# Optimization experiments

Measured on AMD Instinct MI355X. Metric: run time of the kernel, lower is better.

Reference implementation:

```python
import jax, jax.numpy as jnp
import numpy as np

BN_EPS = 1e-3
SLOPE = 0.1
K = 100
CLUSTER_TEMP = 5.0


def setup_inputs() -> dict:
    key = jax.random.key(0)
    ks = jax.random.split(key, 5)
    N, Cin, Cout = 8192, 1, 64
    d = 49 * Cout  # (28/4)^2 * out_channels
    return {
        "x": jax.random.normal(ks[0], (N, Cin, 28, 28), jnp.float32),
        "conv1_w": jax.random.normal(ks[1], (128, Cin, 5, 5), jnp.float32) * 0.05,
        "conv1_b": jnp.zeros((128,), jnp.float32),
        "bn1_gamma": jnp.ones((128,), jnp.float32),
        "bn1_beta": jnp.zeros((128,), jnp.float32),
        "bn1_mean": jnp.zeros((128,), jnp.float32),
        "bn1_var": jnp.ones((128,), jnp.float32),
        "conv2_w": jax.random.normal(ks[2], (Cout, 128, 5, 5), jnp.float32) * 0.02,
        "conv2_b": jnp.zeros((Cout,), jnp.float32),
        "bn2_gamma": jnp.ones((Cout,), jnp.float32),
        "bn2_beta": jnp.zeros((Cout,), jnp.float32),
        "bn2_mean": jnp.zeros((Cout,), jnp.float32),
        "bn2_var": jnp.ones((Cout,), jnp.float32),
        "init_mu": jax.random.uniform(ks[3], (K, d), jnp.float32),
        "num_iter": 10,
    }


def _conv_bn_lrelu(x, w, b, gamma, beta, mean, var):
    # Conv2d(k=5, s=2, p=2) -> BatchNorm (eval/running stats) -> LeakyReLU(0.1)
    h = jax.lax.conv_general_dilated(
        x, w, window_strides=(2, 2), padding=[(2, 2), (2, 2)],
        dimension_numbers=("NCHW", "OIHW", "NCHW"))
    h = h + b[None, :, None, None]
    inv = gamma * jax.lax.rsqrt(var + BN_EPS)
    h = h * inv[None, :, None, None] + (beta - mean * inv)[None, :, None, None]
    return jnp.where(h >= 0, h, SLOPE * h)


def _cluster(data, mu, num_iter):
    # Row L2-normalize (equivalent to diag(1/||row||) @ data)
    data = data / jnp.linalg.norm(data, axis=1, keepdims=True)  # [n, d]
    for _ in range(num_iter):
        dist = data @ mu.T                                 # [n, K]
        r = jax.nn.softmax(CLUSTER_TEMP * dist, axis=1)    # [n, K]
        cluster_r = r.sum(axis=0)                          # [K]
        cluster_mean = r.T @ data                          # [K, d]
        mu = cluster_mean / cluster_r[:, None]
    dist = data @ mu.T
    r = jax.nn.softmax(CLUSTER_TEMP * dist, axis=1)
    return mu, r, dist


def reference(x, conv1_w, conv1_b, bn1_gamma, bn1_beta, bn1_mean, bn1_var,
              conv2_w, conv2_b, bn2_gamma, bn2_beta, bn2_mean, bn2_var,
              init_mu, num_iter):
    h = _conv_bn_lrelu(x, conv1_w, conv1_b, bn1_gamma, bn1_beta, bn1_mean, bn1_var)
    h = _conv_bn_lrelu(h, conv2_w, conv2_b, bn2_gamma, bn2_beta, bn2_mean, bn2_var)
    embeds = h.reshape(h.shape[0], -1)                     # [N, 49*Cout]
    mu_init, _, _ = _cluster(embeds, init_mu, int(num_iter))
    mu, r, dist = _cluster(embeds, jax.lax.stop_gradient(mu_init), 1)
    return mu, r, dist
```

## Files before the change

### kernel.cpp

```cpp
#include <hip/hip_runtime.h>
#include <hip/hip_bf16.h>
#include <math.h>

#define BN_EPS 1e-3f
#define SLOPE  0.1f
#define TEMP   5.0f
#define DDIM   3136
#define DDIMP  3200

typedef __attribute__((ext_vector_type(8))) short bf16x8;
typedef __attribute__((ext_vector_type(4))) float f32x4;

static __device__ __forceinline__ short f2b(float f) {
  __hip_bfloat16 h = __float2bfloat16(f);
  return *reinterpret_cast<short*>(&h);
}

#define W2B_OFF   0u
#define W1B_OFF   102400u
#define DB_OFF    204800u
#define DB_SZ     (8192u*3136u/2u)
#define DT_OFF    (DB_OFF + DB_SZ)
#define DT_SZ     (3200u*8192u/2u)
#define MUB_OFF   (DT_OFF + DT_SZ)
#define MUB_SZ    (112u*3136u/2u)
#define MUF_OFF   (MUB_OFF + MUB_SZ)
#define MUF_SZ    (100u*3136u)
#define CMS_OFF   (MUF_OFF + MUF_SZ)
#define CMS_SZ    (16u*3200u*112u/2u)
#define RT_OFF    (CMS_OFF + CMS_SZ)
#define RT_SZ     (112u*8192u/2u)
#define CR_OFF    (RT_OFF + RT_SZ)

__global__ __launch_bounds__(256) void k_w2b(const float* __restrict__ w2,
                                             __hip_bfloat16* __restrict__ w2b) {
  int idx = blockIdx.x * 256 + threadIdx.x;
  if (idx >= 204800) return;
  int ci   = idx & 31;
  int lr   = (idx >> 5) & 15;
  int rest = idx >> 9;
  int kk   = rest % 100;
  int oct  = rest / 100;
  int oc   = oct * 16 + lr;
  int tap  = kk >> 2;
  int c    = ((kk & 3) << 5) + ci;
  w2b[idx] = __float2bfloat16(w2[(oc * 128 + c) * 25 + tap]);
}

__global__ __launch_bounds__(256) void k_w1b(const float* __restrict__ w1,
                                             __hip_bfloat16* __restrict__ w1b) {
  int idx = blockIdx.x * 256 + threadIdx.x;
  if (idx >= 4096) return;
  int k   = idx & 31;
  int lr  = (idx >> 5) & 15;
  int oct = idx >> 9;
  int oc  = oct * 16 + lr;
  float v = (k < 25) ? w1[oc * 25 + k] : 0.f;
  w1b[idx] = __float2bfloat16(v);
}

__global__ __launch_bounds__(256) void k_conv(
    const float* __restrict__ x,
    const __hip_bfloat16* __restrict__ w1bh, const float* __restrict__ b1,
    const float* __restrict__ g1,  const float* __restrict__ be1,
    const float* __restrict__ mn1, const float* __restrict__ vr1,
    const __hip_bfloat16* __restrict__ w2bh, const float* __restrict__ b2,
    const float* __restrict__ g2,  const float* __restrict__ be2,
    const float* __restrict__ mn2, const float* __restrict__ vr2,
    __hip_bfloat16* __restrict__ db) {
  __shared__ float xs[1024];
  __shared__ float bn2s[128];
  __shared__ float bn1a[128], bn1b[128];
  __shared__ float nrm[4];
  __shared__ __align__(16) __hip_bfloat16 h1s[197 * 128];

  const int t    = threadIdx.x;
  const int img  = blockIdx.x;
  const int lane = t & 63;
  const int wv   = t >> 6;
  const int lr   = lane & 15;
  const int kg   = lane >> 4;
  const short* w2b = (const short*)w2bh;
  const short* w1b = (const short*)w1bh;

  for (int i = t; i < 1024; i += 256) xs[i] = 0.f;
  if (t < 64) {
    float a2 = g2[t] * rsqrtf(vr2[t] + BN_EPS);
    bn2s[t]      = a2;
    bn2s[64 + t] = b2[t] * a2 + be2[t] - mn2[t] * a2;
    ((unsigned*)(h1s + 196 * 128))[t] = 0u;
  }
  if (t < 128) {
    float a1 = g1[t] * rsqrtf(vr1[t] + BN_EPS);
    bn1a[t] = a1;
    bn1b[t] = b1[t] * a1 + be1[t] - mn1[t] * a1;
  }
  __syncthreads();
  const float* xi = x + (size_t)img * 784;
  for (int i = t; i < 784; i += 256) {
    int yy = i / 28, xx = i % 28;
    xs[(yy + 2) * 32 + (xx + 2)] = xi[i];
  }
  __syncthreads();

  {
    bf16x8 a0 = *(const bf16x8*)(w1b + (2 * wv) * 512 + lr * 32 + kg * 8);
    bf16x8 a1 = *(const bf16x8*)(w1b + (2 * wv + 1) * 512 + lr * 32 + kg * 8);
    for (int pt = 0; pt < 13; ++pt) {
      const int px  = pt * 16 + lr;
      const int pxc = (px < 196) ? px : 195;
      const int oy  = pxc / 14, ox = pxc - 14 * (pxc / 14);
      const float* xb = xs + (2 * oy) * 32 + 2 * ox;
      short bs[8];
#pragma unroll
      for (int j = 0; j < 8; ++j) {
        int k   = kg * 8 + j;
        int tap = (k < 25) ? k : 0;
        int kh  = tap / 5, kw = tap - 5 * (tap / 5);
        bs[j] = f2b(xb[kh * 32 + kw]);
      }
      bf16x8 b;
#pragma unroll
      for (int j = 0; j < 8; ++j) b[j] = bs[j];
      f32x4 c0 = {0.f, 0.f, 0.f, 0.f}, c1 = {0.f, 0.f, 0.f, 0.f};
      c0 = __builtin_amdgcn_mfma_f32_16x16x32_bf16(a0, b, c0, 0, 0, 0);
      c1 = __builtin_amdgcn_mfma_f32_16x16x32_bf16(a1, b, c1, 0, 0, 0);
      if (px < 196) {
        const int swz = (px & 7) << 4;
        unsigned w0lo, w0hi, w1lo, w1hi;
        {
          float v[4], u[4];
#pragma unroll
          for (int r = 0; r < 4; ++r) {
            int oc = wv * 32 + kg * 4 + r;
            float h = c0[r] * bn1a[oc] + bn1b[oc];
            v[r] = (h >= 0.f) ? h : SLOPE * h;
            int oc2 = oc + 16;
            float h2 = c1[r] * bn1a[oc2] + bn1b[oc2];
            u[r] = (h2 >= 0.f) ? h2 : SLOPE * h2;
          }
          w0lo = (unsigned)(unsigned short)f2b(v[0]) |
                 ((unsigned)(unsigned short)f2b(v[1]) << 16);
          w0hi = (unsigned)(unsigned short)f2b(v[2]) |
                 ((unsigned)(unsigned short)f2b(v[3]) << 16);
          w1lo = (unsigned)(unsigned short)f2b(u[0]) |
                 ((unsigned)(unsigned short)f2b(u[1]) << 16);
          w1hi = (unsigned)(unsigned short)f2b(u[2]) |
                 ((unsigned)(unsigned short)f2b(u[3]) << 16);
        }
        char* base = (char*)h1s + px * 256;
        const int o0 = ((wv * 32 + kg * 4) * 2) ^ swz;
        const int o1 = ((wv * 32 + 16 + kg * 4) * 2) ^ swz;
        *(uint2*)(base + o0) = make_uint2(w0lo, w0hi);
        *(uint2*)(base + o1) = make_uint2(w1lo, w1hi);
      }
    }
  }
  __syncthreads();

  const int woff  = lr * 32 + kg * 8;
  const int kgoff = kg << 4;
  int pxA[4], oyA[4], oxA[4];
#pragma unroll
  for (int pt = 0; pt < 4; ++pt) {
    int p = pt * 16 + lr;
    pxA[pt] = p;
    oyA[pt] = p / 7;
    oxA[pt] = p - 7 * oyA[pt];
  }

  f32x4 acc[4][4];
#pragma unroll
  for (int oct = 0; oct < 4; ++oct)
#pragma unroll
    for (int pt = 0; pt < 4; ++pt) acc[oct][pt] = (f32x4){0.f, 0.f, 0.f, 0.f};

  const int s0 = 25 * wv, s1e = s0 + 25;
  int curtap = -1;
  int rowB[4], rowS[4];

  auto loadk = [&](int kk, bf16x8* areg, bf16x8* breg) {
    int tap = kk >> 2;
    if (tap != curtap) {
      curtap = tap;
      int kh = tap / 5, kw = tap - 5 * (tap / 5);
#pragma unroll
      for (int pt = 0; pt < 4; ++pt) {
        int iy = 2 * oyA[pt] - 2 + kh;
        int ix = 2 * oxA[pt] - 2 + kw;
        bool val = (pxA[pt] < 49) & ((unsigned)iy < 14u) & ((unsigned)ix < 14u);
        int ip = val ? iy * 14 + ix : 196;
        rowB[pt] = ip * 256;
        rowS[pt] = (ip & 7) << 4;
      }
    }
    int c01 = (kk & 3) << 6;
#pragma unroll
    for (int oct = 0; oct < 4; ++oct)
      areg[oct] = *(const bf16x8*)(w2b + ((oct * 100 + kk) << 9) + woff);
#pragma unroll
    for (int pt = 0; pt < 4; ++pt)
      breg[pt] = *(const bf16x8*)((const char*)h1s + rowB[pt] +
                                  ((c01 | kgoff) ^ rowS[pt]));
  };

  bf16x8 a[4], b[4], an[4], bn_[4];
  loadk(s0, a, b);
  for (int kk = s0; kk < s1e; ++kk) {
    if (kk + 1 < s1e) loadk(kk + 1, an, bn_);
#pragma unroll
    for (int oct = 0; oct < 4; ++oct)
#pragma unroll
      for (int pt = 0; pt < 4; ++pt)
        acc[oct][pt] = __builtin_amdgcn_mfma_f32_16x16x32_bf16(a[oct], b[pt],
                                                               acc[oct][pt], 0, 0, 0);
#pragma unroll
    for (int q = 0; q < 4; ++q) { a[q] = an[q]; b[q] = bn_[q]; }
  }
  __syncthreads();

  float* red = (float*)h1s;
  if (wv != 0) {
#pragma unroll
    for (int oct = 0; oct < 4; ++oct)
#pragma unroll
      for (int pt = 0; pt < 4; ++pt)
#pragma unroll
        for (int r = 0; r < 4; ++r)
          red[(wv - 1) * 4096 + ((oct * 4 + pt) * 4 + r) * 64 + lane] =
              acc[oct][pt][r];
  }
  __syncthreads();
  if (wv == 0) {
#pragma unroll
    for (int oct = 0; oct < 4; ++oct)
#pragma unroll
      for (int pt = 0; pt < 4; ++pt)
#pragma unroll
        for (int r = 0; r < 4; ++r) {
          const int i = (oct * 4 + pt) * 4 + r;
          float v = acc[oct][pt][r] + red[i * 64 + lane] +
                    red[4096 + i * 64 + lane] + red[8192 + i * 64 + lane];
          red[i * 64 + lane] = v;
        }
  }
  __syncthreads();

  float outv[16];
  float ss = 0.f;
#pragma unroll
  for (int pt = 0; pt < 4; ++pt) {
#pragma unroll
    for (int r = 0; r < 4; ++r) {
      const int i = ((wv * 4 + pt) * 4 + r);
      float v = red[i * 64 + lane];
      const int oc = wv * 16 + kg * 4 + r;
      v = v * bn2s[oc] + bn2s[64 + oc];
      v = (v >= 0.f) ? v : SLOPE * v;
      outv[pt * 4 + r] = v;
      if (pxA[pt] < 49) ss += v * v;
    }
  }
#pragma unroll
  for (int m = 1; m < 64; m <<= 1) ss += __shfl_xor(ss, m, 64);
  if (lane == 0) nrm[wv] = ss;
  __syncthreads();
  const float invn = rsqrtf(nrm[0] + nrm[1] + nrm[2] + nrm[3]);
  __hip_bfloat16* dro = db + (size_t)img * DDIM;
#pragma unroll
  for (int pt = 0; pt < 4; ++pt) {
    if (pxA[pt] < 49) {
#pragma unroll
      for (int r = 0; r < 4; ++r) {
        const int oc = wv * 16 + kg * 4 + r;
        dro[oc * 49 + pxA[pt]] = __float2bfloat16(outv[pt * 4 + r] * invn);
      }
    }
  }
}

__global__ __launch_bounds__(256) void k_tr(const __hip_bfloat16* __restrict__ dbh,
                                            __hip_bfloat16* __restrict__ dTh) {
  __shared__ short tile[64][72];
  const int t   = threadIdx.x;
  const int i   = t >> 2;
  const int seg = t & 3;
  const size_t img0 = (size_t)blockIdx.x * 64;
  const size_t d0   = (size_t)blockIdx.y * 64;
  const short* src = (const short*)dbh + (img0 + i) * DDIM + d0 + seg * 16;
  bf16x8 v0 = *(const bf16x8*)src;
  bf16x8 v1 = *(const bf16x8*)(src + 8);
  *(bf16x8*)&tile[i][seg * 16]     = v0;
  *(bf16x8*)&tile[i][seg * 16 + 8] = v1;
  __syncthreads();
  short tmp[16];
#pragma unroll
  for (int k = 0; k < 16; ++k) tmp[k] = tile[seg * 16 + k][i];
  short* dst = (short*)dTh + (d0 + i) * 8192 + img0 + seg * 16;
  *(bf16x8*)dst       = *(bf16x8*)tmp;
  *(bf16x8*)(dst + 8) = *((bf16x8*)tmp + 1);
}

__global__ __launch_bounds__(256) void k_muinit(const float* __restrict__ mu0,
                                                __hip_bfloat16* __restrict__ mub) {
  int idx = blockIdx.x * 256 + threadIdx.x;
  if (idx >= 112 * DDIM) return;
  int j = idx / DDIM, d = idx - j * DDIM;
  float v = (j < 100) ? mu0[j * DDIM + d] : 0.f;
  mub[idx] = __float2bfloat16(v);
}

__global__ __launch_bounds__(512) void k_dsm(
    const __hip_bfloat16* __restrict__ data,
    const __hip_bfloat16* __restrict__ mu,
    __hip_bfloat16* __restrict__ rT,
    float* __restrict__ cr,
    float* __restrict__ outr,
    float* __restrict__ outd,
    int final_flag) {
  __shared__ float red[8][64][29];
  const int t    = threadIdx.x;
  const int lane = t & 63;
  const int wv   = t >> 6;
  const int rg   = wv >> 2;
  const int ks   = wv & 3;
  const int rowbase = blockIdx.x * 32;
  const int s0 = (98 * ks) >> 2;
  const int s1 = (98 * (ks + 1)) >> 2;
  const int lr = lane & 15;
  const int kg = lane >> 4;

  const __hip_bfloat16* arow = data + (size_t)(rowbase + rg * 16 + lr) * DDIM + kg * 8;
  const __hip_bfloat16* brow = mu + (size_t)lr * DDIM + kg * 8;

  f32x4 acc[7];
#pragma unroll
  for (int i = 0; i < 7; ++i) acc[i] = (f32x4){0.f, 0.f, 0.f, 0.f};

  bf16x8 a, b[7], an, bn_[7];
  {
    const int k0 = s0 * 32;
    a = *(const bf16x8*)(arow + k0);
#pragma unroll
    for (int tl = 0; tl < 7; ++tl)
      b[tl] = *(const bf16x8*)(brow + (size_t)tl * 16 * DDIM + k0);
  }
  for (int s = s0; s < s1; ++s) {
    if (s + 1 < s1) {
      const int k1 = (s + 1) * 32;
      an = *(const bf16x8*)(arow + k1);
#pragma unroll
      for (int tl = 0; tl < 7; ++tl)
        bn_[tl] = *(const bf16x8*)(brow + (size_t)tl * 16 * DDIM + k1);
    }
#pragma unroll
    for (int tl = 0; tl < 7; ++tl)
      acc[tl] = __builtin_amdgcn_mfma_f32_16x16x32_bf16(a, b[tl], acc[tl], 0, 0, 0);
    a = an;
#pragma unroll
    for (int tl = 0; tl < 7; ++tl) b[tl] = bn_[tl];
  }

#pragma unroll
  for (int tl = 0; tl < 7; ++tl)
#pragma unroll
    for (int r = 0; r < 4; ++r) red[wv][lane][tl * 4 + r] = acc[tl][r];
  __syncthreads();

  const int r_   = lane >> 4;
  const int kg_t = wv & 3;
  const int rg_t = wv >> 2;
  const int grow = rowbase + 4 * wv + r_;
  float v[7];
#pragma unroll
  for (int tl = 0; tl < 7; ++tl) {
    float s = 0.f;
#pragma unroll
    for (int k2 = 0; k2 < 4; ++k2)
      s += red[rg_t * 4 + k2][kg_t * 16 + lr][tl * 4 + r_];
    v[tl] = s;
  }

  if (final_flag) {
#pragma unroll
    for (int tl = 0; tl < 7; ++tl) {
      const int col = tl * 16 + lr;
      if (col < 100) outd[(size_t)grow * 100 + col] = v[tl];
    }
  }

  float m = -1e30f;
#pragma unroll
  for (int tl = 0; tl < 7; ++tl) {
    const bool valid = (tl < 6) || (lr < 4);
    m = fmaxf(m, valid ? v[tl] : -1e30f);
  }
  m = fmaxf(m, __shfl_xor(m, 1, 64));
  m = fmaxf(m, __shfl_xor(m, 2, 64));
  m = fmaxf(m, __shfl_xor(m, 4, 64));
  m = fmaxf(m, __shfl_xor(m, 8, 64));
  float e[7];
  float s = 0.f;
#pragma unroll
  for (int tl = 0; tl < 7; ++tl) {
    const bool valid = (tl < 6) || (lr < 4);
    e[tl] = valid ? __expf(TEMP * (v[tl] - m)) : 0.f;
    s += e[tl];
  }
  s += __shfl_xor(s, 1, 64);
  s += __shfl_xor(s, 2, 64);
  s += __shfl_xor(s, 4, 64);
  s += __shfl_xor(s, 8, 64);
  const float inv = 1.f / s;
#pragma unroll
  for (int tl = 0; tl < 7; ++tl) e[tl] *= inv;

  if (final_flag) {
#pragma unroll
    for (int tl = 0; tl < 7; ++tl) {
      const int col = tl * 16 + lr;
      if (col < 100) outr[(size_t)grow * 100 + col] = e[tl];
    }
    return;
  }

#pragma unroll
  for (int tl = 0; tl < 7; ++tl) {
    const int col = tl * 16 + lr;
    if (col < 100)
      rT[(size_t)col * 8192 + grow] = __float2bfloat16(e[tl]);
  }
  float cs[7];
#pragma unroll
  for (int tl = 0; tl < 7; ++tl) {
    float c2 = e[tl];
    c2 += __shfl_xor(c2, 16, 64);
    c2 += __shfl_xor(c2, 32, 64);
    cs[tl] = c2;
  }
  if (lane < 16) {
#pragma unroll
    for (int tl = 0; tl < 7; ++tl) {
      const int col = tl * 16 + lane;
      if (col < 100) atomicAdd(cr + col, cs[tl]);
    }
  }
}

__global__ __launch_bounds__(256) void k_mu(
    const __hip_bfloat16* __restrict__ dataT,
    const __hip_bfloat16* __restrict__ rT,
    __hip_bfloat16* __restrict__ cms) {
  const int t    = threadIdx.x;
  const int lane = t & 63;
  const int wv   = t >> 6;
  const int mbase = blockIdx.x * 128 + wv * 32;
  const int kbase = blockIdx.y * 512;
  const int lr = lane & 15;
  const int kg = lane >> 4;

  const __hip_bfloat16* arow0 = dataT + (size_t)(mbase + lr) * 8192 + kbase + kg * 8;
  const __hip_bfloat16* arow1 = arow0 + (size_t)16 * 8192;
  const __hip_bfloat16* brow  = rT + (size_t)lr * 8192 + kbase + kg * 8;

  f32x4 acc[2][7];
#pragma unroll
  for (int mt = 0; mt < 2; ++mt)
#pragma unroll
    for (int i = 0; i < 7; ++i) acc[mt][i] = (f32x4){0.f, 0.f, 0.f, 0.f};

  bf16x8 a0, a1, b[7], a0n, a1n, bn_[7];
  a0 = *(const bf16x8*)(arow0);
  a1 = *(const bf16x8*)(arow1);
#pragma unroll
  for (int tl = 0; tl < 7; ++tl)
    b[tl] = *(const bf16x8*)(brow + (size_t)tl * 16 * 8192);
  for (int s = 0; s < 16; ++s) {
    if (s + 1 < 16) {
      const int k1 = (s + 1) * 32;
      a0n = *(const bf16x8*)(arow0 + k1);
      a1n = *(const bf16x8*)(arow1 + k1);
#pragma unroll
      for (int tl = 0; tl < 7; ++tl)
        bn_[tl] = *(const bf16x8*)(brow + (size_t)tl * 16 * 8192 + k1);
    }
#pragma unroll
    for (int tl = 0; tl < 7; ++tl) {
      acc[0][tl] = __builtin_amdgcn_mfma_f32_16x16x32_bf16(a0, b[tl], acc[0][tl], 0, 0, 0);
      acc[1][tl] = __builtin_amdgcn_mfma_f32_16x16x32_bf16(a1, b[tl], acc[1][tl], 0, 0, 0);
    }
    a0 = a0n; a1 = a1n;
#pragma unroll
    for (int tl = 0; tl < 7; ++tl) b[tl] = bn_[tl];
  }

  __hip_bfloat16* dst = cms + (size_t)blockIdx.y * (3200u * 112u);
#pragma unroll
  for (int mt = 0; mt < 2; ++mt) {
#pragma unroll
    for (int tl = 0; tl < 7; ++tl) {
      const int col = tl * 16 + lr;
#pragma unroll
      for (int r = 0; r < 4; ++r)
        dst[(size_t)(mbase + mt * 16 + kg * 4 + r) * 112 + col] =
            __float2bfloat16(acc[mt][tl][r]);
    }
  }
}

__global__ __launch_bounds__(256) void k_upd(const __hip_bfloat16* __restrict__ cms,
                                             const float* __restrict__ cr,
                                             float* __restrict__ muf,
                                             __hip_bfloat16* __restrict__ mub) {
  __shared__ float tile[16][113];
  const int t  = threadIdx.x;
  const int d0 = blockIdx.x * 16;
  for (int e = t; e < 16 * 112; e += 256) {
    int dd = e / 112, jj = e - dd * 112;
    const __hip_bfloat16* p = cms + (size_t)(d0 + dd) * 112 + jj;
    float v = 0.f;
#pragma unroll
    for (int s2 = 0; s2 < 16; ++s2)
      v += __bfloat162float(p[(size_t)s2 * (3200u * 112u)]);
    tile[dd][jj] = v;
  }
  __syncthreads();
  for (int e = t; e < 100 * 16; e += 256) {
    int jj = e >> 4, dd = e & 15;
    float v = tile[dd][jj] / cr[jj];
    muf[(size_t)jj * DDIM + d0 + dd] = v;
    mub[(size_t)jj * DDIM + d0 + dd] = __float2bfloat16(v);
  }
}

extern "C" void kernel_launch(void* const* d_in, const int* in_sizes, int n_in,
                              void* d_out, int out_size, void* d_ws, size_t ws_size,
                              hipStream_t stream) {
  const float* x   = (const float*)d_in[0];
  const float* w1  = (const float*)d_in[1];
  const float* b1  = (const float*)d_in[2];
  const float* g1  = (const float*)d_in[3];
  const float* be1 = (const float*)d_in[4];
  const float* mn1 = (const float*)d_in[5];
  const float* vr1 = (const float*)d_in[6];
  const float* w2  = (const float*)d_in[7];
  const float* b2  = (const float*)d_in[8];
  const float* g2  = (const float*)d_in[9];
  const float* be2 = (const float*)d_in[10];
  const float* mn2 = (const float*)d_in[11];
  const float* vr2 = (const float*)d_in[12];
  const float* mu0 = (const float*)d_in[13];

  float* ws = (float*)d_ws;
  __hip_bfloat16* w2b = (__hip_bfloat16*)(ws + W2B_OFF);
  __hip_bfloat16* w1b = (__hip_bfloat16*)(ws + W1B_OFF);
  __hip_bfloat16* db  = (__hip_bfloat16*)(ws + DB_OFF);
  __hip_bfloat16* dT  = (__hip_bfloat16*)(ws + DT_OFF);
  __hip_bfloat16* mub = (__hip_bfloat16*)(ws + MUB_OFF);
  float*          muf = ws + MUF_OFF;
  __hip_bfloat16* cms = (__hip_bfloat16*)(ws + CMS_OFF);
  __hip_bfloat16* rT  = (__hip_bfloat16*)(ws + RT_OFF);
  float*          crb = ws + CR_OFF;
  float*          out = (float*)d_out;

  k_w2b<<<800, 256, 0, stream>>>(w2, w2b);
  k_w1b<<<16, 256, 0, stream>>>(w1, w1b);
  k_conv<<<8192, 256, 0, stream>>>(x, w1b, b1, g1, be1, mn1, vr1,
                                   w2b, b2, g2, be2, mn2, vr2, db);
  k_tr<<<dim3(128, 49), 256, 0, stream>>>(db, dT);
  k_muinit<<<(112 * DDIM + 255) / 256, 256, 0, stream>>>(mu0, mub);
  hipMemsetAsync(rT + (size_t)100 * 8192, 0, 12 * 8192 * sizeof(__hip_bfloat16),
                 stream);
  hipMemsetAsync(crb, 0, 12 * 128 * sizeof(float), stream);

  for (int it = 0; it < 11; ++it) {
    float* cr = crb + it * 128;
    k_dsm<<<256, 512, 0, stream>>>(db, mub, rT, cr, nullptr, nullptr, 0);
    k_mu<<<dim3(25, 16), 256, 0, stream>>>(dT, rT, cms);
    k_upd<<<196, 256, 0, stream>>>(cms, cr, muf, mub);
  }

  k_dsm<<<256, 512, 0, stream>>>(db, mub, rT, crb + 11 * 128,
                                 out + 313600, out + 1132800, 1);
  hipMemcpyAsync(out, muf, (size_t)MUF_SZ * sizeof(float),
                 hipMemcpyDeviceToDevice, stream);
}
```

Before: 1.932 ms.

## Fuse clustering iterations into one cooperative persistent kernel with grid syncs

Replaces the 34 per-iteration launches of the distance/softmax, cluster-mean and update kernels with a single cooperative kernel of 256 blocks × 512 threads that uses grid.sync between phases. The cluster-mean phase is reshaped to 250 blocks, each wave computing one 16-row tile over a larger K chunk, and the K split drops from 16 partial sums to 10. The goal is to remove launch overhead and shrink the partial-sum buffer and its reduction. In exchange, each phase runs at the occupancy fixed by the fused kernel, some blocks sit idle in phases B and C, and grid-wide barriers add their own cost.

```diff
diff --git a/kernel.cpp b/kernel.cpp
--- a/kernel.cpp
+++ b/kernel.cpp
@@ -1,12 +1,14 @@
 #include <hip/hip_runtime.h>
 #include <hip/hip_bf16.h>
+#include <hip/hip_cooperative_groups.h>
 #include <math.h>
+
+namespace cg = cooperative_groups;
 
 #define BN_EPS 1e-3f
 #define SLOPE  0.1f
 #define TEMP   5.0f
 #define DDIM   3136
-#define DDIMP  3200
 
 typedef __attribute__((ext_vector_type(8))) short bf16x8;
 typedef __attribute__((ext_vector_type(4))) float f32x4;
@@ -27,7 +29,7 @@
 #define MUF_OFF   (MUB_OFF + MUB_SZ)
 #define MUF_SZ    (100u*3136u)
 #define CMS_OFF   (MUF_OFF + MUF_SZ)
-#define CMS_SZ    (16u*3200u*112u/2u)
+#define CMS_SZ    (10u*3200u*112u/2u)
 #define RT_OFF    (CMS_OFF + CMS_SZ)
 #define RT_SZ     (112u*8192u/2u)
 #define CR_OFF    (RT_OFF + RT_SZ)
@@ -310,15 +312,12 @@
   mub[idx] = __float2bfloat16(v);
 }
 
-__global__ __launch_bounds__(512) void k_dsm(
+__device__ __forceinline__ void phaseA(
     const __hip_bfloat16* __restrict__ data,
     const __hip_bfloat16* __restrict__ mu,
-    __hip_bfloat16* __restrict__ rT,
-    float* __restrict__ cr,
-    float* __restrict__ outr,
-    float* __restrict__ outd,
-    int final_flag) {
-  __shared__ float red[8][64][29];
+    __hip_bfloat16* __restrict__ rT, float* __restrict__ cr,
+    float* __restrict__ outr, float* __restrict__ outd,
+    int final_flag, float (*red)[64][29]) {
   const int t    = threadIdx.x;
   const int lane = t & 63;
   const int wv   = t >> 6;
@@ -421,116 +420,136 @@
       const int col = tl * 16 + lr;
       if (col < 100) outr[(size_t)grow * 100 + col] = e[tl];
     }
-    return;
-  }
-
-#pragma unroll
-  for (int tl = 0; tl < 7; ++tl) {
-    const int col = tl * 16 + lr;
-    if (col < 100)
-      rT[(size_t)col * 8192 + grow] = __float2bfloat16(e[tl]);
-  }
-  float cs[7];
-#pragma unroll
-  for (int tl = 0; tl < 7; ++tl) {
-    float c2 = e[tl];
-    c2 += __shfl_xor(c2, 16, 64);
-    c2 += __shfl_xor(c2, 32, 64);
-    cs[tl] = c2;
-  }
-  if (lane < 16) {
+  } else {
 #pragma unroll
     for (int tl = 0; tl < 7; ++tl) {
-      const int col = tl * 16 + lane;
-      if (col < 100) atomicAdd(cr + col, cs[tl]);
-    }
-  }
-}
-
-__global__ __launch_bounds__(256) void k_mu(
-    const __hip_bfloat16* __restrict__ dataT,
-    const __hip_bfloat16* __restrict__ rT,
-    __hip_bfloat16* __restrict__ cms) {
+      const int col = tl * 16 + lr;
+      if (col < 100)
+        rT[(size_t)col * 8192 + grow] = __float2bfloat16(e[tl]);
+    }
+    float cs[7];
+#pragma unroll
+    for (int tl = 0; tl < 7; ++tl) {
+      float c2 = e[tl];
+      c2 += __shfl_xor(c2, 16, 64);
+      c2 += __shfl_xor(c2, 32, 64);
+      cs[tl] = c2;
+    }
+    if (lane < 16) {
+#pragma unroll
+      for (int tl = 0; tl < 7; ++tl) {
+        const int col = tl * 16 + lane;
+        if (col < 100) atomicAdd(cr + col, cs[tl]);
+      }
+    }
+  }
+}
+
+__device__ __forceinline__ void phaseB(const __hip_bfloat16* __restrict__ dataT,
+                                       const __hip_bfloat16* __restrict__ rT,
+                                       __hip_bfloat16* __restrict__ cms) {
+  const int bid = blockIdx.x;
+  if (bid >= 250) return;
+  const int mb = bid / 10, kc = bid % 10;
+  const int step0 = (kc < 6) ? kc * 26 : 156 + (kc - 6) * 25;
+  const int nst   = (kc < 6) ? 26 : 25;
+  const int kbase = step0 * 32;
+
   const int t    = threadIdx.x;
   const int lane = t & 63;
   const int wv   = t >> 6;
-  const int mbase = blockIdx.x * 128 + wv * 32;
-  const int kbase = blockIdx.y * 512;
+  const int mbase = mb * 128 + wv * 16;
   const int lr = lane & 15;
   const int kg = lane >> 4;
 
-  const __hip_bfloat16* arow0 = dataT + (size_t)(mbase + lr) * 8192 + kbase + kg * 8;
-  const __hip_bfloat16* arow1 = arow0 + (size_t)16 * 8192;
-  const __hip_bfloat16* brow  = rT + (size_t)lr * 8192 + kbase + kg * 8;
-
-  f32x4 acc[2][7];
-#pragma unroll
-  for (int mt = 0; mt < 2; ++mt)
-#pragma unroll
-    for (int i = 0; i < 7; ++i) acc[mt][i] = (f32x4){0.f, 0.f, 0.f, 0.f};
-
-  bf16x8 a0, a1, b[7], a0n, a1n, bn_[7];
-  a0 = *(const bf16x8*)(arow0);
-  a1 = *(const bf16x8*)(arow1);
+  const __hip_bfloat16* arow = dataT + (size_t)(mbase + lr) * 8192 + kbase + kg * 8;
+  const __hip_bfloat16* brow = rT + (size_t)lr * 8192 + kbase + kg * 8;
+
+  f32x4 acc[7];
+#pragma unroll
+  for (int i = 0; i < 7; ++i) acc[i] = (f32x4){0.f, 0.f, 0.f, 0.f};
+
+  bf16x8 a, b[7], an, bn_[7];
+  a = *(const bf16x8*)(arow);
 #pragma unroll
   for (int tl = 0; tl < 7; ++tl)
     b[tl] = *(const bf16x8*)(brow + (size_t)tl * 16 * 8192);
-  for (int s = 0; s < 16; ++s) {
-    if (s + 1 < 16) {
+  for (int s = 0; s < nst; ++s) {
+    if (s + 1 < nst) {
       const int k1 = (s + 1) * 32;
-      a0n = *(const bf16x8*)(arow0 + k1);
-      a1n = *(const bf16x8*)(arow1 + k1);
+      an = *(const bf16x8*)(arow + k1);
 #pragma unroll
       for (int tl = 0; tl < 7; ++tl)
         bn_[tl] = *(const bf16x8*)(brow + (size_t)tl * 16 * 8192 + k1);
     }
 #pragma unroll
-    for (int tl = 0; tl < 7; ++tl) {
-      acc[0][tl] = __builtin_amdgcn_mfma_f32_16x16x32_bf16(a0, b[tl], acc[0][tl], 0, 0, 0);
-      acc[1][tl] = __builtin_amdgcn_mfma_f32_16x16x32_bf16(a1, b[tl], acc[1][tl], 0, 0, 0);
-    }
-    a0 = a0n; a1 = a1n;
+    for (int tl = 0; tl < 7; ++tl)
+      acc[tl] = __builtin_amdgcn_mfma_f32_16x16x32_bf16(a, b[tl], acc[tl], 0, 0, 0);
+    a = an;
 #pragma unroll
     for (int tl = 0; tl < 7; ++tl) b[tl] = bn_[tl];
   }
 
-  __hip_bfloat16* dst = cms + (size_t)blockIdx.y * (3200u * 112u);
-#pragma unroll
-  for (int mt = 0; mt < 2; ++mt) {
-#pragma unroll
-    for (int tl = 0; tl < 7; ++tl) {
-      const int col = tl * 16 + lr;
-#pragma unroll
-      for (int r = 0; r < 4; ++r)
-        dst[(size_t)(mbase + mt * 16 + kg * 4 + r) * 112 + col] =
-            __float2bfloat16(acc[mt][tl][r]);
-    }
-  }
-}
-
-__global__ __launch_bounds__(256) void k_upd(const __hip_bfloat16* __restrict__ cms,
-                                             const float* __restrict__ cr,
-                                             float* __restrict__ muf,
-                                             __hip_bfloat16* __restrict__ mub) {
-  __shared__ float tile[16][113];
+  __hip_bfloat16* dst = cms + (size_t)kc * (3200u * 112u);
+#pragma unroll
+  for (int tl = 0; tl < 7; ++tl) {
+    const int col = tl * 16 + lr;
+#pragma unroll
+    for (int r = 0; r < 4; ++r)
+      dst[(size_t)(mbase + kg * 4 + r) * 112 + col] = __float2bfloat16(acc[tl][r]);
+  }
+}
+
+__device__ __forceinline__ void phaseC(const __hip_bfloat16* __restrict__ cms,
+                                       const float* __restrict__ cr,
+                                       float* __restrict__ muf,
+                                       __hip_bfloat16* __restrict__ mub,
+                                       float (*tile)[113]) {
+  if (blockIdx.x >= 196) return;
   const int t  = threadIdx.x;
   const int d0 = blockIdx.x * 16;
-  for (int e = t; e < 16 * 112; e += 256) {
+  for (int e = t; e < 16 * 112; e += 512) {
     int dd = e / 112, jj = e - dd * 112;
     const __hip_bfloat16* p = cms + (size_t)(d0 + dd) * 112 + jj;
     float v = 0.f;
 #pragma unroll
-    for (int s2 = 0; s2 < 16; ++s2)
+    for (int s2 = 0; s2 < 10; ++s2)
       v += __bfloat162float(p[(size_t)s2 * (3200u * 112u)]);
     tile[dd][jj] = v;
   }
   __syncthreads();
-  for (int e = t; e < 100 * 16; e += 256) {
+  for (int e = t; e < 100 * 16; e += 512) {
     int jj = e >> 4, dd = e & 15;
     float v = tile[dd][jj] / cr[jj];
     muf[(size_t)jj * DDIM + d0 + dd] = v;
     mub[(size_t)jj * DDIM + d0 + dd] = __float2bfloat16(v);
   }
+}
+
+__global__ __launch_bounds__(512) void k_cluster(
+    const __hip_bfloat16* __restrict__ db,
+    const __hip_bfloat16* __restrict__ dT,
+    __hip_bfloat16* __restrict__ mub,
+    float* __restrict__ muf,
+    __hip_bfloat16* __restrict__ cms,
+    __hip_bfloat16* __restrict__ rT,
+    float* __restrict__ crb,
+    float* __restrict__ outr,
+    float* __restrict__ outd) {
+  cg::grid_group grid = cg::this_grid();
+  __shared__ float red[8][64][29];
+  for (int it = 0; it < 11; ++it) {
+    phaseA(db, mub, rT, crb + it * 128, nullptr, nullptr, 0, red);
+    __threadfence();
+    grid.sync();
+    phaseB(dT, rT, cms);
+    __threadfence();
+    grid.sync();
+    phaseC(cms, crb + it * 128, muf, mub, (float(*)[113])red);
+    __threadfence();
+    grid.sync();
+  }
+  phaseA(db, mub, rT, crb + 11 * 128, outr, outd, 1, red);
 }
 
 extern "C" void kernel_launch(void* const* d_in, const int* in_sizes, int n_in,
@@ -573,15 +592,14 @@
                  stream);
   hipMemsetAsync(crb, 0, 12 * 128 * sizeof(float), stream);
 
-  for (int it = 0; it < 11; ++it) {
-    float* cr = crb + it * 128;
-    k_dsm<<<256, 512, 0, stream>>>(db, mub, rT, cr, nullptr, nullptr, 0);
-    k_mu<<<dim3(25, 16), 256, 0, stream>>>(dT, rT, cms);
-    k_upd<<<196, 256, 0, stream>>>(cms, cr, muf, mub);
-  }
-
-  k_dsm<<<256, 512, 0, stream>>>(db, mub, rT, crb + 11 * 128,
-                                 out + 313600, out + 1132800, 1);
+  float* outr = out + 313600;
+  float* outd = out + 1132800;
+  void* args[] = {(void*)&db, (void*)&dT, (void*)&mub, (void*)&muf,
+                  (void*)&cms, (void*)&rT, (void*)&crb,
+                  (void*)&outr, (void*)&outd};
+  hipLaunchCooperativeKernel((void*)k_cluster, dim3(256), dim3(512),
+                             args, 0, stream);
+
   hipMemcpyAsync(out, muf, (size_t)MUF_SZ * sizeof(float),
                  hipMemcpyDeviceToDevice, stream);
 }
```

Result: slower. 4.449 ms (+130.3%).

## Fuse cluster-mean GEMM with mu update via in-block split-K reduction

Applied to the files above, without the earlier changes.

Replaces the split-K k_mu kernel, which wrote bf16 partial sums to a workspace, and the separate k_upd reduce/normalize kernel with one k_mu2 kernel. In k_mu2 eight waves each cover a K-slice, reduce through shared memory, divide by cluster responsibility and write mu directly, with the final iteration writing fp32 output in place of a trailing memcpy. Weight prep kernels and the memsets are also merged into fewer launches. This removes the partial-sum round trip and several launches per iteration. In exchange there are only 196 blocks with one 16-row tile each, so parallelism and per-block register reuse are lower.

```diff
diff --git a/kernel.cpp b/kernel.cpp
--- a/kernel.cpp
+++ b/kernel.cpp
@@ -6,7 +6,6 @@
 #define SLOPE  0.1f
 #define TEMP   5.0f
 #define DDIM   3136
-#define DDIMP  3200
 
 typedef __attribute__((ext_vector_type(8))) short bf16x8;
 typedef __attribute__((ext_vector_type(4))) float f32x4;
@@ -21,42 +20,39 @@
 #define DB_OFF    204800u
 #define DB_SZ     (8192u*3136u/2u)
 #define DT_OFF    (DB_OFF + DB_SZ)
-#define DT_SZ     (3200u*8192u/2u)
+#define DT_SZ     (8192u*3136u/2u)
 #define MUB_OFF   (DT_OFF + DT_SZ)
 #define MUB_SZ    (112u*3136u/2u)
-#define MUF_OFF   (MUB_OFF + MUB_SZ)
-#define MUF_SZ    (100u*3136u)
-#define CMS_OFF   (MUF_OFF + MUF_SZ)
-#define CMS_SZ    (16u*3200u*112u/2u)
-#define RT_OFF    (CMS_OFF + CMS_SZ)
+#define RT_OFF    (MUB_OFF + MUB_SZ)
 #define RT_SZ     (112u*8192u/2u)
 #define CR_OFF    (RT_OFF + RT_SZ)
 
-__global__ __launch_bounds__(256) void k_w2b(const float* __restrict__ w2,
-                                             __hip_bfloat16* __restrict__ w2b) {
+__global__ __launch_bounds__(256) void k_wprep(const float* __restrict__ w2,
+                                               const float* __restrict__ w1,
+                                               __hip_bfloat16* __restrict__ w2b,
+                                               __hip_bfloat16* __restrict__ w1b) {
   int idx = blockIdx.x * 256 + threadIdx.x;
-  if (idx >= 204800) return;
-  int ci   = idx & 31;
-  int lr   = (idx >> 5) & 15;
-  int rest = idx >> 9;
-  int kk   = rest % 100;
-  int oct  = rest / 100;
-  int oc   = oct * 16 + lr;
-  int tap  = kk >> 2;
-  int c    = ((kk & 3) << 5) + ci;
-  w2b[idx] = __float2bfloat16(w2[(oc * 128 + c) * 25 + tap]);
-}
-
-__global__ __launch_bounds__(256) void k_w1b(const float* __restrict__ w1,
-                                             __hip_bfloat16* __restrict__ w1b) {
-  int idx = blockIdx.x * 256 + threadIdx.x;
-  if (idx >= 4096) return;
-  int k   = idx & 31;
-  int lr  = (idx >> 5) & 15;
-  int oct = idx >> 9;
-  int oc  = oct * 16 + lr;
-  float v = (k < 25) ? w1[oc * 25 + k] : 0.f;
-  w1b[idx] = __float2bfloat16(v);
+  if (idx < 204800) {
+    int ci   = idx & 31;
+    int lr   = (idx >> 5) & 15;
+    int rest = idx >> 9;
+    int kk   = rest % 100;
+    int oct  = rest / 100;
+    int oc   = oct * 16 + lr;
+    int tap  = kk >> 2;
+    int c    = ((kk & 3) << 5) + ci;
+    w2b[idx] = __float2bfloat16(w2[(oc * 128 + c) * 25 + tap]);
+  } else {
+    int j = idx - 204800;
+    if (j < 4096) {
+      int k   = j & 31;
+      int lr  = (j >> 5) & 15;
+      int oct = j >> 9;
+      int oc  = oct * 16 + lr;
+      float v = (k < 25) ? w1[oc * 25 + k] : 0.f;
+      w1b[j] = __float2bfloat16(v);
+    }
+  }
 }
 
 __global__ __launch_bounds__(256) void k_conv(
@@ -302,12 +298,18 @@
 }
 
 __global__ __launch_bounds__(256) void k_muinit(const float* __restrict__ mu0,
-                                                __hip_bfloat16* __restrict__ mub) {
+                                                __hip_bfloat16* __restrict__ mub,
+                                                __hip_bfloat16* __restrict__ rT,
+                                                float* __restrict__ crb) {
   int idx = blockIdx.x * 256 + threadIdx.x;
-  if (idx >= 112 * DDIM) return;
-  int j = idx / DDIM, d = idx - j * DDIM;
-  float v = (j < 100) ? mu0[j * DDIM + d] : 0.f;
-  mub[idx] = __float2bfloat16(v);
+  if (idx < 112 * DDIM) {
+    int j = idx / DDIM, d = idx - j * DDIM;
+    float v = (j < 100) ? mu0[j * DDIM + d] : 0.f;
+    mub[idx] = __float2bfloat16(v);
+  }
+  if (idx < 12 * 8192)
+    rT[(size_t)100 * 8192 + idx] = __float2bfloat16(0.f);
+  if (idx < 12 * 128) crb[idx] = 0.f;
 }
 
 __global__ __launch_bounds__(512) void k_dsm(
@@ -447,89 +449,79 @@
   }
 }
 
-__global__ __launch_bounds__(256) void k_mu(
+__global__ __launch_bounds__(512) void k_mu2(
     const __hip_bfloat16* __restrict__ dataT,
     const __hip_bfloat16* __restrict__ rT,
-    __hip_bfloat16* __restrict__ cms) {
+    const float* __restrict__ cr,
+    float* __restrict__ mufo,
+    __hip_bfloat16* __restrict__ mub) {
+  __shared__ float red[8][64][29];
   const int t    = threadIdx.x;
   const int lane = t & 63;
   const int wv   = t >> 6;
-  const int mbase = blockIdx.x * 128 + wv * 32;
-  const int kbase = blockIdx.y * 512;
+  const int mbase = blockIdx.x * 16;
   const int lr = lane & 15;
   const int kg = lane >> 4;
-
-  const __hip_bfloat16* arow0 = dataT + (size_t)(mbase + lr) * 8192 + kbase + kg * 8;
-  const __hip_bfloat16* arow1 = arow0 + (size_t)16 * 8192;
-  const __hip_bfloat16* brow  = rT + (size_t)lr * 8192 + kbase + kg * 8;
-
-  f32x4 acc[2][7];
-#pragma unroll
-  for (int mt = 0; mt < 2; ++mt)
-#pragma unroll
-    for (int i = 0; i < 7; ++i) acc[mt][i] = (f32x4){0.f, 0.f, 0.f, 0.f};
-
-  bf16x8 a0, a1, b[7], a0n, a1n, bn_[7];
-  a0 = *(const bf16x8*)(arow0);
-  a1 = *(const bf16x8*)(arow1);
+  const int kbase = wv * 1024;
+
+  const __hip_bfloat16* arow = dataT + (size_t)(mbase + lr) * 8192 + kbase + kg * 8;
+  const __hip_bfloat16* brow = rT + (size_t)lr * 8192 + kbase + kg * 8;
+
+  f32x4 acc[7];
+#pragma unroll
+  for (int i = 0; i < 7; ++i) acc[i] = (f32x4){0.f, 0.f, 0.f, 0.f};
+
+  bf16x8 a, b[7], an, bn_[7];
+  a = *(const bf16x8*)(arow);
 #pragma unroll
   for (int tl = 0; tl < 7; ++tl)
     b[tl] = *(const bf16x8*)(brow + (size_t)tl * 16 * 8192);
-  for (int s = 0; s < 16; ++s) {
-    if (s + 1 < 16) {
+  for (int s = 0; s < 32; ++s) {
+    if (s + 1 < 32) {
       const int k1 = (s + 1) * 32;
-      a0n = *(const bf16x8*)(arow0 + k1);
-      a1n = *(const bf16x8*)(arow1 + k1);
+      an = *(const bf16x8*)(arow + k1);
 #pragma unroll
       for (int tl = 0; tl < 7; ++tl)
         bn_[tl] = *(const bf16x8*)(brow + (size_t)tl * 16 * 8192 + k1);
     }
 #pragma unroll
-    for (int tl = 0; tl < 7; ++tl) {
-      acc[0][tl] = __builtin_amdgcn_mfma_f32_16x16x32_bf16(a0, b[tl], acc[0][tl], 0, 0, 0);
-      acc[1][tl] = __builtin_amdgcn_mfma_f32_16x16x32_bf16(a1, b[tl], acc[1][tl], 0, 0, 0);
-    }
-    a0 = a0n; a1 = a1n;
+    for (int tl = 0; tl < 7; ++tl)
+      acc[tl] = __builtin_amdgcn_mfma_f32_16x16x32_bf16(a, b[tl], acc[tl], 0, 0, 0);
+    a = an;
 #pragma unroll
     for (int tl = 0; tl < 7; ++tl) b[tl] = bn_[tl];
   }
 
-  __hip_bfloat16* dst = cms + (size_t)blockIdx.y * (3200u * 112u);
-#pragma unroll
-  for (int mt = 0; mt < 2; ++mt) {
-#pragma unroll
-    for (int tl = 0; tl < 7; ++tl) {
-      const int col = tl * 16 + lr;
-#pragma unroll
-      for (int r = 0; r < 4; ++r)
-        dst[(size_t)(mbase + mt * 16 + kg * 4 + r) * 112 + col] =
-            __float2bfloat16(acc[mt][tl][r]);
-    }
-  }
-}
-
-__global__ __launch_bounds__(256) void k_upd(const __hip_bfloat16* __restrict__ cms,
-                                             const float* __restrict__ cr,
-                                             float* __restrict__ muf,
-                                             __hip_bfloat16* __restrict__ mub) {
-  __shared__ float tile[16][113];
-  const int t  = threadIdx.x;
-  const int d0 = blockIdx.x * 16;
-  for (int e = t; e < 16 * 112; e += 256) {
-    int dd = e / 112, jj = e - dd * 112;
-    const __hip_bfloat16* p = cms + (size_t)(d0 + dd) * 112 + jj;
-    float v = 0.f;
-#pragma unroll
-    for (int s2 = 0; s2 < 16; ++s2)
-      v += __bfloat162float(p[(size_t)s2 * (3200u * 112u)]);
-    tile[dd][jj] = v;
-  }
-  __syncthreads();
-  for (int e = t; e < 100 * 16; e += 256) {
-    int jj = e >> 4, dd = e & 15;
-    float v = tile[dd][jj] / cr[jj];
-    muf[(size_t)jj * DDIM + d0 + dd] = v;
-    mub[(size_t)jj * DDIM + d0 + dd] = __float2bfloat16(v);
+#pragma unroll
+  for (int tl = 0; tl < 7; ++tl)
+#pragma unroll
+    for (int r = 0; r < 4; ++r) red[wv][lane][tl * 4 + r] = acc[tl][r];
+  __syncthreads();
+
+  if (wv >= 7) return;
+  const int tl = wv;
+  const int col = tl * 16 + lr;
+  float vv[4];
+#pragma unroll
+  for (int r = 0; r < 4; ++r) {
+    float s2 = 0.f;
+#pragma unroll
+    for (int k2 = 0; k2 < 8; ++k2) s2 += red[k2][lane][tl * 4 + r];
+    vv[r] = s2;
+  }
+  if (col < 100) {
+    const float inv = 1.f / cr[col];
+#pragma unroll
+    for (int r = 0; r < 4; ++r) vv[r] *= inv;
+    const int d0 = mbase + kg * 4;
+    unsigned lo = (unsigned)(unsigned short)f2b(vv[0]) |
+                  ((unsigned)(unsigned short)f2b(vv[1]) << 16);
+    unsigned hi = (unsigned)(unsigned short)f2b(vv[2]) |
+                  ((unsigned)(unsigned short)f2b(vv[3]) << 16);
+    *(uint2*)((short*)mub + (size_t)col * DDIM + d0) = make_uint2(lo, hi);
+    if (mufo)
+      *(float4*)(mufo + (size_t)col * DDIM + d0) =
+          make_float4(vv[0], vv[1], vv[2], vv[3]);
   }
 }
 
@@ -557,31 +549,23 @@
   __hip_bfloat16* db  = (__hip_bfloat16*)(ws + DB_OFF);
   __hip_bfloat16* dT  = (__hip_bfloat16*)(ws + DT_OFF);
   __hip_bfloat16* mub = (__hip_bfloat16*)(ws + MUB_OFF);
-  float*          muf = ws + MUF_OFF;
-  __hip_bfloat16* cms = (__hip_bfloat16*)(ws + CMS_OFF);
   __hip_bfloat16* rT  = (__hip_bfloat16*)(ws + RT_OFF);
   float*          crb = ws + CR_OFF;
   float*          out = (float*)d_out;
 
-  k_w2b<<<800, 256, 0, stream>>>(w2, w2b);
-  k_w1b<<<16, 256, 0, stream>>>(w1, w1b);
+  k_wprep<<<816, 256, 0, stream>>>(w2, w1, w2b, w1b);
   k_conv<<<8192, 256, 0, stream>>>(x, w1b, b1, g1, be1, mn1, vr1,
                                    w2b, b2, g2, be2, mn2, vr2, db);
   k_tr<<<dim3(128, 49), 256, 0, stream>>>(db, dT);
-  k_muinit<<<(112 * DDIM + 255) / 256, 256, 0, stream>>>(mu0, mub);
-  hipMemsetAsync(rT + (size_t)100 * 8192, 0, 12 * 8192 * sizeof(__hip_bfloat16),
-                 stream);
-  hipMemsetAsync(crb, 0, 12 * 128 * sizeof(float), stream);
+  k_muinit<<<(112 * DDIM + 255) / 256, 256, 0, stream>>>(mu0, mub, rT, crb);
 
   for (int it = 0; it < 11; ++it) {
-    float* cr = crb + it * 128;
-    k_dsm<<<256, 512, 0, stream>>>(db, mub, rT, cr, nullptr, nullptr, 0);
-    k_mu<<<dim3(25, 16), 256, 0, stream>>>(dT, rT, cms);
-    k_upd<<<196, 256, 0, stream>>>(cms, cr, muf, mub);
+    k_dsm<<<256, 512, 0, stream>>>(db, mub, rT, crb + it * 128,
+                                   nullptr, nullptr, 0);
+    k_mu2<<<196, 512, 0, stream>>>(dT, rT, crb + it * 128,
+                                   (it == 10) ? out : nullptr, mub);
   }
 
   k_dsm<<<256, 512, 0, stream>>>(db, mub, rT, crb + 11 * 128,
                                  out + 313600, out + 1132800, 1);
-  hipMemcpyAsync(out, muf, (size_t)MUF_SZ * sizeof(float),
-                 hipMemcpyDeviceToDevice, stream);
-}
+}
```

New measurement: 2.120 ms. +9.7%, slower.
